# Kernel optimization log

Measured on AMD Instinct MI355X. Metric: run time of the kernel, lower is better.

## Reference

```python
import jax, jax.numpy as jnp
import numpy as np

NEG_INF = -9e15  # matches the torch module's zero_vec constant
ALPHA = 0.2      # LeakyReLU negative slope


def setup_inputs() -> dict:
    key = jax.random.key(0)
    k1, k2, k3, k4, k5, k6 = jax.random.split(key, 6)
    N_t, N_o, F_in, F_out = 8192, 8192, 256, 64
    return {
        "t_input": jax.random.normal(k1, (N_t, F_in), dtype=jnp.float32),
        "o_input": jax.random.normal(k2, (N_o, F_in), dtype=jnp.float32),
        "W_t": jax.random.normal(k3, (F_in, F_out), dtype=jnp.float32) * 0.1,
        "W_o": jax.random.normal(k4, (F_in, F_out), dtype=jnp.float32) * 0.1,
        "a": jax.random.normal(k5, (2 * F_out, 1), dtype=jnp.float32) * 0.1,
        "adj": jax.random.randint(k6, (N_t, N_o), 0, 2, dtype=jnp.int32),
    }


def reference(t_input, o_input, W_t, W_o, a, adj):
    # Linear projections
    h_t = t_input @ W_t            # [N_t, F]
    h_o = o_input @ W_o            # [N_o, F]
    F_out = h_t.shape[1]
    a_t = a[:F_out, 0]             # [F]
    a_o = a[F_out:, 0]             # [F]
    # e[i,j] = leakyrelu(cat(h_t[i], h_o[j]) . a) = leakyrelu(h_t[i].a_t + h_o[j].a_o)
    # (avoids materializing the N_t*N_o*2F concat tensor; same math)
    e = jax.nn.leaky_relu(
        (h_t @ a_t)[:, None] + (h_o @ a_o)[None, :], negative_slope=ALPHA
    )                              # [N_t, N_o]
    attention = jnp.where(adj > 0, e, NEG_INF)
    attention = jax.nn.softmax(attention, axis=1)
    # dropout is identity at eval time
    h_prime = attention @ h_o      # [N_t, F]
    return jax.nn.elu(h_prime)     # concat=True
```

## Files before the change

### kernel.cpp

```cpp
#include <hip/hip_runtime.h>
#include <math.h>

#define NT 8192
#define NO 8192
#define FIN 256
#define FOUT 64
#define SPLIT 8
#define JSP (NO/SPLIT)
#define ROWT 64

#define OFF_ST  ((size_t)0)
#define OFF_SO  (OFF_ST + (size_t)NT)
#define OFF_WT  (OFF_SO + (size_t)NO)
#define OFF_WO  (OFF_WT + (size_t)FIN)
#define OFF_NUM (OFF_WO + (size_t)FIN)
#define OFF_DEN (OFF_NUM + (size_t)SPLIT*NT*FOUT)
#define OFF_HOB (OFF_DEN + (size_t)SPLIT*NT)
#define OFF_MSK (OFF_HOB + (size_t)NO*FOUT/2)

typedef __attribute__((ext_vector_type(8))) short short8;
typedef __attribute__((ext_vector_type(4))) float float4v;

static __device__ __forceinline__ unsigned short f2bf(float x) {
  unsigned int u = __float_as_uint(x);
  unsigned int r = (u + 0x7fffu + ((u >> 16) & 1u)) >> 16;
  return (unsigned short)r;
}
static __device__ __forceinline__ int pk2(float a, float b) {
  return (int)((unsigned int)f2bf(a) | ((unsigned int)f2bf(b) << 16));
}
static __device__ __forceinline__ float bflo(int p) {
  return __uint_as_float(((unsigned int)p) << 16);
}
static __device__ __forceinline__ float bfhi(int p) {
  return __uint_as_float(((unsigned int)p) & 0xffff0000u);
}

__global__ void k_wvec(const float* __restrict__ Wt, const float* __restrict__ Wo,
                       const float* __restrict__ a, float* __restrict__ ws) {
  int t = threadIdx.x;
  float s1 = 0.f, s2 = 0.f;
#pragma unroll
  for (int fq = 0; fq < FOUT/4; ++fq) {
    float4 wt4 = *(const float4*)(Wt + (size_t)t*FOUT + fq*4);
    float4 wo4 = *(const float4*)(Wo + (size_t)t*FOUT + fq*4);
    float4 at4 = *(const float4*)(a + fq*4);
    float4 ao4 = *(const float4*)(a + FOUT + fq*4);
    s1 += wt4.x*at4.x + wt4.y*at4.y + wt4.z*at4.z + wt4.w*at4.w;
    s2 += wo4.x*ao4.x + wo4.y*ao4.y + wo4.z*ao4.z + wo4.w*ao4.w;
  }
  ws[OFF_WT + t] = s1;
  ws[OFF_WO + t] = s2;
}

__global__ void k_prep(const float* __restrict__ tin, const float* __restrict__ oin,
                       const float* __restrict__ Wo, const float* __restrict__ a,
                       float* __restrict__ ws) {
  int b = blockIdx.x, t = threadIdx.x;
  int wv = t >> 6, lane = t & 63;
  {
    float4 w = ((const float4*)(ws + OFF_WT))[lane];
#pragma unroll
    for (int r = 0; r < 4; ++r) {
      int row = b*16 + wv*4 + r;
      float4 v = ((const float4*)(tin + (size_t)row*FIN))[lane];
      float p = v.x*w.x + v.y*w.y + v.z*w.z + v.w*w.w;
#pragma unroll
      for (int m = 32; m >= 1; m >>= 1) p += __shfl_xor(p, m, 64);
      if (lane == 0) ws[OFF_ST + row] = p;
    }
  }
  {
    unsigned short* hobp = (unsigned short*)(ws + OFF_HOB);
    int r0 = b*16 + wv*4;
    const float* ob = oin + (size_t)r0 * FIN;
    float acc[4];
#pragma unroll
    for (int r = 0; r < 4; ++r) acc[r] = 0.f;
#pragma unroll 2
    for (int k = 0; k < FIN; k += 4) {
      float w0 = Wo[(size_t)(k+0)*FOUT + lane];
      float w1 = Wo[(size_t)(k+1)*FOUT + lane];
      float w2 = Wo[(size_t)(k+2)*FOUT + lane];
      float w3 = Wo[(size_t)(k+3)*FOUT + lane];
#pragma unroll
      for (int r = 0; r < 4; ++r) {
        float4 ov = *(const float4*)(ob + (size_t)r*FIN + k);
        acc[r] = fmaf(ov.x, w0, acc[r]);
        acc[r] = fmaf(ov.y, w1, acc[r]);
        acc[r] = fmaf(ov.z, w2, acc[r]);
        acc[r] = fmaf(ov.w, w3, acc[r]);
      }
    }
    float ao = a[FOUT + lane];
    int fg = lane >> 4, n16 = lane & 15;
#pragma unroll
    for (int r = 0; r < 4; ++r) {
      int j = r0 + r;
      int jt = j >> 5, jl = j & 31;
      int ldst = (jl >> 3) * 16 + n16;
      int e = jl & 7;
      hobp[(((size_t)jt*4 + fg)*64 + ldst)*8 + e] = f2bf(acc[r]);
      float p = acc[r] * ao;
#pragma unroll
      for (int m = 32; m >= 1; m >>= 1) p += __shfl_xor(p, m, 64);
      if (lane == 0) ws[OFF_SO + j] = p;
    }
  }
}

__global__ void k_mask(const int* __restrict__ adj, float* __restrict__ ws) {
  unsigned int* mw = (unsigned int*)(ws + OFF_MSK);
  int wv = threadIdx.x >> 6, lane = threadIdx.x & 63;
  int i = blockIdx.x * 4 + wv;
  const int* ar = adj + (size_t)i*NO;
#pragma unroll 4
  for (int jg = 0; jg < NO/64; ++jg) {
    int v = ar[jg*64 + lane];
    unsigned long long m = __ballot(v > 0);
    if (lane == 0) {
      mw[(size_t)(2*jg)  *NT + i] = (unsigned int)m;
      mw[(size_t)(2*jg+1)*NT + i] = (unsigned int)(m >> 32);
    }
  }
}

__launch_bounds__(256, 4)
__global__ void k_attn(float* __restrict__ ws) {
  const float* st = ws + OFF_ST;
  const float* so = ws + OFF_SO;
  const unsigned int* mT = (const unsigned int*)(ws + OFF_MSK);
  const unsigned short* hobp = (const unsigned short*)(ws + OFF_HOB);
  float* gnum = ws + OFF_NUM;
  float* gden = ws + OFF_DEN;

  int t = threadIdx.x, b = blockIdx.x;
  int wv = t >> 6, lane = t & 63;
  int s  = b & (SPLIT - 1);
  int bi = b >> 3;
  int i0 = bi * ROWT;
  int jb = s * JSP;

  int rsrc = lane >> 2, csrc = lane & 3;
  int irow_s = i0 + wv*16 + rsrc;
  float sti = st[irow_s];

  const unsigned int* mrow = mT + (size_t)(jb >> 5)*NT + irow_s;
  const float* sop = so + jb + csrc*8;
  const unsigned short* hpb = hobp + (size_t)(jb >> 5)*2048 + lane*8;

  int r16 = lane & 15, kg = lane >> 4;
  int sidx4 = ((r16 * 4 + kg) << 2);

  float4v acc0 = (float4v)0.f, acc1 = (float4v)0.f;
  float4v acc2 = (float4v)0.f, acc3 = (float4v)0.f;
  float dsum = 0.f;

#pragma unroll 2
  for (int tt = 0; tt < JSP/32; ++tt) {
    unsigned int mwv = mrow[(size_t)tt*NT];
    float4 s0 = *(const float4*)(sop + tt*32);
    float4 s1 = *(const float4*)(sop + tt*32 + 4);
    const unsigned short* hb = hpb + (size_t)tt*2048;
    short8 b0 = *(const short8*)(hb);
    short8 b1 = *(const short8*)(hb + 512);
    short8 b2 = *(const short8*)(hb + 1024);
    short8 b3 = *(const short8*)(hb + 1536);

    unsigned int msh = mwv >> (csrc * 8);
    float x0 = sti + s0.x; x0 = fmaxf(x0, 0.2f*x0);
    float x1 = sti + s0.y; x1 = fmaxf(x1, 0.2f*x1);
    float x2 = sti + s0.z; x2 = fmaxf(x2, 0.2f*x2);
    float x3 = sti + s0.w; x3 = fmaxf(x3, 0.2f*x3);
    float x4 = sti + s1.x; x4 = fmaxf(x4, 0.2f*x4);
    float x5 = sti + s1.y; x5 = fmaxf(x5, 0.2f*x5);
    float x6 = sti + s1.z; x6 = fmaxf(x6, 0.2f*x6);
    float x7 = sti + s1.w; x7 = fmaxf(x7, 0.2f*x7);
    float w0 = (msh & 1u)   ? __expf(x0) : 0.f;
    float w1 = (msh & 2u)   ? __expf(x1) : 0.f;
    float w2 = (msh & 4u)   ? __expf(x2) : 0.f;
    float w3 = (msh & 8u)   ? __expf(x3) : 0.f;
    float w4 = (msh & 16u)  ? __expf(x4) : 0.f;
    float w5 = (msh & 32u)  ? __expf(x5) : 0.f;
    float w6 = (msh & 64u)  ? __expf(x6) : 0.f;
    float w7 = (msh & 128u) ? __expf(x7) : 0.f;

    int p0 = pk2(w0, w1);
    int p1 = pk2(w2, w3);
    int p2 = pk2(w4, w5);
    int p3 = pk2(w6, w7);
    dsum += bflo(p0) + bfhi(p0) + bflo(p1) + bfhi(p1)
          + bflo(p2) + bfhi(p2) + bflo(p3) + bfhi(p3);

    int4 ai;
    ai.x = __builtin_amdgcn_ds_bpermute(sidx4, p0);
    ai.y = __builtin_amdgcn_ds_bpermute(sidx4, p1);
    ai.z = __builtin_amdgcn_ds_bpermute(sidx4, p2);
    ai.w = __builtin_amdgcn_ds_bpermute(sidx4, p3);
    short8 afrag = *(short8*)&ai;

    acc0 = __builtin_amdgcn_mfma_f32_16x16x32_bf16(afrag, b0, acc0, 0, 0, 0);
    acc1 = __builtin_amdgcn_mfma_f32_16x16x32_bf16(afrag, b1, acc1, 0, 0, 0);
    acc2 = __builtin_amdgcn_mfma_f32_16x16x32_bf16(afrag, b2, acc2, 0, 0, 0);
    acc3 = __builtin_amdgcn_mfma_f32_16x16x32_bf16(afrag, b3, acc3, 0, 0, 0);
  }

  dsum += __shfl_xor(dsum, 1, 64);
  dsum += __shfl_xor(dsum, 2, 64);
  if (csrc == 0) gden[(size_t)s*NT + i0 + wv*16 + rsrc] = dsum;

  size_t obase = ((size_t)s*NT + i0 + wv*16 + kg*4) * FOUT + r16;
#pragma unroll
  for (int r = 0; r < 4; ++r) {
    gnum[obase + (size_t)r*FOUT +  0] = acc0[r];
    gnum[obase + (size_t)r*FOUT + 16] = acc1[r];
    gnum[obase + (size_t)r*FOUT + 32] = acc2[r];
    gnum[obase + (size_t)r*FOUT + 48] = acc3[r];
  }
}

__global__ void k_comb(const float* __restrict__ ws, float* __restrict__ out) {
  int idx = blockIdx.x * 256 + threadIdx.x;
  int i = idx >> 6;
  float num = 0.f, den = 0.f;
#pragma unroll
  for (int s = 0; s < SPLIT; ++s) {
    num += ws[OFF_NUM + ((size_t)s*NT + i)*FOUT + (idx & 63)];
    den += ws[OFF_DEN + (size_t)s*NT + i];
  }
  float r = num / den;
  out[idx] = (r > 0.f) ? r : (__expf(r) - 1.f);
}

extern "C" void kernel_launch(void* const* d_in, const int* in_sizes, int n_in,
                              void* d_out, int out_size, void* d_ws, size_t ws_size,
                              hipStream_t stream) {
  const float* tin = (const float*)d_in[0];
  const float* oin = (const float*)d_in[1];
  const float* Wt  = (const float*)d_in[2];
  const float* Wo  = (const float*)d_in[3];
  const float* a   = (const float*)d_in[4];
  const int*   adj = (const int*)d_in[5];
  float* out = (float*)d_out;
  float* ws  = (float*)d_ws;

  hipLaunchKernelGGL(k_wvec, dim3(1),              dim3(256), 0, stream, Wt, Wo, a, ws);
  hipLaunchKernelGGL(k_mask, dim3(NT/4),           dim3(256), 0, stream, adj, ws);
  hipLaunchKernelGGL(k_prep, dim3(NT/16),          dim3(256), 0, stream, tin, oin, Wo, a, ws);
  hipLaunchKernelGGL(k_attn, dim3(NT/ROWT*SPLIT),  dim3(256), 0, stream, ws);
  hipLaunchKernelGGL(k_comb, dim3(NT*FOUT/256),    dim3(256), 0, stream, ws, out);
}
```

Baseline: 502.2 us.

## Fuse adjacency mask packing into attention kernel and drop bpermute shuffles

Removes the separate mask-packing kernel and the W·a vector kernel. The attention kernel now ballots its own adjacency tile into an LDS bitmask, and k_prep computes W_t·a_t per block. The weight-generation lane layout is changed so each lane produces the MFMA A-fragment directly, which removes the four ds_bpermute ops per iteration. This avoids writing and re-reading the packed mask through global memory and saves two launches. In exchange, each attention block does a serial 16-row adjacency read before its compute loop, with no overlap against the MFMA work.

```diff
diff --git a/kernel.cpp b/kernel.cpp
--- a/kernel.cpp
+++ b/kernel.cpp
@@ -9,14 +9,11 @@
 #define JSP (NO/SPLIT)
 #define ROWT 64
 
-#define OFF_ST  ((size_t)0)
-#define OFF_SO  (OFF_ST + (size_t)NT)
-#define OFF_WT  (OFF_SO + (size_t)NO)
-#define OFF_WO  (OFF_WT + (size_t)FIN)
-#define OFF_NUM (OFF_WO + (size_t)FIN)
+#define OFF_NUM ((size_t)0)
 #define OFF_DEN (OFF_NUM + (size_t)SPLIT*NT*FOUT)
-#define OFF_HOB (OFF_DEN + (size_t)SPLIT*NT)
-#define OFF_MSK (OFF_HOB + (size_t)NO*FOUT/2)
+#define OFF_SO  (OFF_DEN + (size_t)SPLIT*NT)
+#define OFF_ST  (OFF_SO + (size_t)NO)
+#define OFF_HOB (OFF_ST + (size_t)NT)
 
 typedef __attribute__((ext_vector_type(8))) short short8;
 typedef __attribute__((ext_vector_type(4))) float float4v;
@@ -36,30 +33,25 @@
   return __uint_as_float(((unsigned int)p) & 0xffff0000u);
 }
 
-__global__ void k_wvec(const float* __restrict__ Wt, const float* __restrict__ Wo,
+__global__ void k_prep(const float* __restrict__ tin, const float* __restrict__ oin,
+                       const float* __restrict__ Wt, const float* __restrict__ Wo,
                        const float* __restrict__ a, float* __restrict__ ws) {
-  int t = threadIdx.x;
-  float s1 = 0.f, s2 = 0.f;
-#pragma unroll
-  for (int fq = 0; fq < FOUT/4; ++fq) {
-    float4 wt4 = *(const float4*)(Wt + (size_t)t*FOUT + fq*4);
-    float4 wo4 = *(const float4*)(Wo + (size_t)t*FOUT + fq*4);
-    float4 at4 = *(const float4*)(a + fq*4);
-    float4 ao4 = *(const float4*)(a + FOUT + fq*4);
-    s1 += wt4.x*at4.x + wt4.y*at4.y + wt4.z*at4.z + wt4.w*at4.w;
-    s2 += wo4.x*ao4.x + wo4.y*ao4.y + wo4.z*ao4.z + wo4.w*ao4.w;
-  }
-  ws[OFF_WT + t] = s1;
-  ws[OFF_WO + t] = s2;
-}
-
-__global__ void k_prep(const float* __restrict__ tin, const float* __restrict__ oin,
-                       const float* __restrict__ Wo, const float* __restrict__ a,
-                       float* __restrict__ ws) {
+  __shared__ float wt_l[FIN];
   int b = blockIdx.x, t = threadIdx.x;
   int wv = t >> 6, lane = t & 63;
   {
-    float4 w = ((const float4*)(ws + OFF_WT))[lane];
+    float s1 = 0.f;
+#pragma unroll
+    for (int fq = 0; fq < FOUT/4; ++fq) {
+      float4 w4 = *(const float4*)(Wt + (size_t)t*FOUT + fq*4);
+      float4 a4 = *(const float4*)(a + fq*4);
+      s1 += w4.x*a4.x + w4.y*a4.y + w4.z*a4.z + w4.w*a4.w;
+    }
+    wt_l[t] = s1;
+  }
+  __syncthreads();
+  {
+    float4 w = ((const float4*)wt_l)[lane];
 #pragma unroll
     for (int r = 0; r < 4; ++r) {
       int row = b*16 + wv*4 + r;
@@ -109,27 +101,11 @@
   }
 }
 
-__global__ void k_mask(const int* __restrict__ adj, float* __restrict__ ws) {
-  unsigned int* mw = (unsigned int*)(ws + OFF_MSK);
-  int wv = threadIdx.x >> 6, lane = threadIdx.x & 63;
-  int i = blockIdx.x * 4 + wv;
-  const int* ar = adj + (size_t)i*NO;
-#pragma unroll 4
-  for (int jg = 0; jg < NO/64; ++jg) {
-    int v = ar[jg*64 + lane];
-    unsigned long long m = __ballot(v > 0);
-    if (lane == 0) {
-      mw[(size_t)(2*jg)  *NT + i] = (unsigned int)m;
-      mw[(size_t)(2*jg+1)*NT + i] = (unsigned int)(m >> 32);
-    }
-  }
-}
-
 __launch_bounds__(256, 4)
-__global__ void k_attn(float* __restrict__ ws) {
+__global__ void k_attn(const int* __restrict__ adj, float* __restrict__ ws) {
+  __shared__ unsigned int msk[4][16][33];
   const float* st = ws + OFF_ST;
   const float* so = ws + OFF_SO;
-  const unsigned int* mT = (const unsigned int*)(ws + OFF_MSK);
   const unsigned short* hobp = (const unsigned short*)(ws + OFF_HOB);
   float* gnum = ws + OFF_NUM;
   float* gden = ws + OFF_DEN;
@@ -141,16 +117,27 @@
   int i0 = bi * ROWT;
   int jb = s * JSP;
 
-  int rsrc = lane >> 2, csrc = lane & 3;
-  int irow_s = i0 + wv*16 + rsrc;
-  float sti = st[irow_s];
-
-  const unsigned int* mrow = mT + (size_t)(jb >> 5)*NT + irow_s;
-  const float* sop = so + jb + csrc*8;
+  {
+    const int* ab = adj + (size_t)(i0 + wv*16)*NO + jb + lane;
+#pragma unroll 1
+    for (int row = 0; row < 16; ++row) {
+      const int* ar = ab + (size_t)row*NO;
+#pragma unroll 4
+      for (int g = 0; g < 16; ++g) {
+        int v = ar[g*64];
+        unsigned long long m = __ballot(v > 0);
+        if (lane == 0) {
+          msk[wv][row][2*g]   = (unsigned int)m;
+          msk[wv][row][2*g+1] = (unsigned int)(m >> 32);
+        }
+      }
+    }
+  }
+
+  int r16 = lane & 15, kg = lane >> 4;
+  float sti = st[i0 + wv*16 + r16];
+  const float* sop = so + jb + kg*8;
   const unsigned short* hpb = hobp + (size_t)(jb >> 5)*2048 + lane*8;
-
-  int r16 = lane & 15, kg = lane >> 4;
-  int sidx4 = ((r16 * 4 + kg) << 2);
 
   float4v acc0 = (float4v)0.f, acc1 = (float4v)0.f;
   float4v acc2 = (float4v)0.f, acc3 = (float4v)0.f;
@@ -158,7 +145,7 @@
 
 #pragma unroll 2
   for (int tt = 0; tt < JSP/32; ++tt) {
-    unsigned int mwv = mrow[(size_t)tt*NT];
+    unsigned int msh = msk[wv][r16][tt] >> (kg*8);
     float4 s0 = *(const float4*)(sop + tt*32);
     float4 s1 = *(const float4*)(sop + tt*32 + 4);
     const unsigned short* hb = hpb + (size_t)tt*2048;
@@ -167,7 +154,6 @@
     short8 b2 = *(const short8*)(hb + 1024);
     short8 b3 = *(const short8*)(hb + 1536);
 
-    unsigned int msh = mwv >> (csrc * 8);
     float x0 = sti + s0.x; x0 = fmaxf(x0, 0.2f*x0);
     float x1 = sti + s0.y; x1 = fmaxf(x1, 0.2f*x1);
     float x2 = sti + s0.z; x2 = fmaxf(x2, 0.2f*x2);
@@ -192,11 +178,7 @@
     dsum += bflo(p0) + bfhi(p0) + bflo(p1) + bfhi(p1)
           + bflo(p2) + bfhi(p2) + bflo(p3) + bfhi(p3);
 
-    int4 ai;
-    ai.x = __builtin_amdgcn_ds_bpermute(sidx4, p0);
-    ai.y = __builtin_amdgcn_ds_bpermute(sidx4, p1);
-    ai.z = __builtin_amdgcn_ds_bpermute(sidx4, p2);
-    ai.w = __builtin_amdgcn_ds_bpermute(sidx4, p3);
+    int4 ai = {p0, p1, p2, p3};
     short8 afrag = *(short8*)&ai;
 
     acc0 = __builtin_amdgcn_mfma_f32_16x16x32_bf16(afrag, b0, acc0, 0, 0, 0);
@@ -205,9 +187,9 @@
     acc3 = __builtin_amdgcn_mfma_f32_16x16x32_bf16(afrag, b3, acc3, 0, 0, 0);
   }
 
-  dsum += __shfl_xor(dsum, 1, 64);
-  dsum += __shfl_xor(dsum, 2, 64);
-  if (csrc == 0) gden[(size_t)s*NT + i0 + wv*16 + rsrc] = dsum;
+  dsum += __shfl_xor(dsum, 16, 64);
+  dsum += __shfl_xor(dsum, 32, 64);
+  if (lane < 16) gden[(size_t)s*NT + i0 + wv*16 + lane] = dsum;
 
   size_t obase = ((size_t)s*NT + i0 + wv*16 + kg*4) * FOUT + r16;
 #pragma unroll
@@ -244,9 +226,7 @@
   float* out = (float*)d_out;
   float* ws  = (float*)d_ws;
 
-  hipLaunchKernelGGL(k_wvec, dim3(1),              dim3(256), 0, stream, Wt, Wo, a, ws);
-  hipLaunchKernelGGL(k_mask, dim3(NT/4),           dim3(256), 0, stream, adj, ws);
-  hipLaunchKernelGGL(k_prep, dim3(NT/16),          dim3(256), 0, stream, tin, oin, Wo, a, ws);
-  hipLaunchKernelGGL(k_attn, dim3(NT/ROWT*SPLIT),  dim3(256), 0, stream, ws);
+  hipLaunchKernelGGL(k_prep, dim3(NT/16),          dim3(256), 0, stream, tin, oin, Wt, Wo, a, ws);
+  hipLaunchKernelGGL(k_attn, dim3(NT/ROWT*SPLIT),  dim3(256), 0, stream, adj, ws);
   hipLaunchKernelGGL(k_comb, dim3(NT*FOUT/256),    dim3(256), 0, stream, ws, out);
 }
```

Result: slower. 528.0 us (+5.1%).
